# Kernel optimization log

Hardware: AMD Instinct MI355X
Metric: run time of the kernel (lower is better)

The kernel has to match this reference:

```python
import jax, jax.numpy as jnp
import numpy as np

N_NODES = 100000


def gcn_layer(x, W, b, src, dst, norm, n):
    # x: [N, Fin] -> linear transform then normalized scatter-add aggregation
    h = x @ W                                   # [N, Fout]
    msgs = h[src] * norm[:, None]               # [E+N, Fout] edge messages
    out = jax.ops.segment_sum(msgs, dst, num_segments=n)
    return out + b


def _build_graph(edge_index, n):
    # add self loops (PyG GCNConv default)
    loops = jnp.arange(n, dtype=edge_index.dtype)
    src = jnp.concatenate([edge_index[0], loops])
    dst = jnp.concatenate([edge_index[1], loops])
    deg = jax.ops.segment_sum(jnp.ones_like(dst, dtype=jnp.float32), dst, num_segments=n)
    dis = jnp.where(deg > 0, jax.lax.rsqrt(deg), 0.0)  # deg^{-1/2}
    norm = dis[src] * dis[dst]                  # symmetric normalization per edge
    return src, dst, norm


def setup_inputs() -> dict:
    key = jax.random.key(0)
    ks = jax.random.split(key, 8)
    x = jax.random.normal(ks[0], (N_NODES, 3), dtype=jnp.float32)
    edge_index = jax.random.randint(ks[1], (2, 6400000), 0, N_NODES, dtype=jnp.int32)
    def glorot(k, fin, fout):
        s = jnp.sqrt(6.0 / (fin + fout))
        return jax.random.uniform(k, (fin, fout), jnp.float32, -s, s)
    return {
        "x": x,
        "edge_index": edge_index,
        "W1": glorot(ks[2], 3, 32), "b1": jnp.zeros((32,), jnp.float32),
        "W2": glorot(ks[3], 32, 32), "b2": jnp.zeros((32,), jnp.float32),
        "W3": glorot(ks[4], 32, 1), "b3": jnp.zeros((1,), jnp.float32),
    }


def reference(x, edge_index, W1, b1, W2, b2, W3, b3):
    n = x.shape[0]
    src, dst, norm = _build_graph(edge_index, n)
    h = jax.nn.relu(gcn_layer(x, W1, b1, src, dst, norm, n))
    h = jax.nn.relu(gcn_layer(h, W2, b2, src, dst, norm, n))
    return gcn_layer(h, W3, b3, src, dst, norm, n)
```

## Files before the change

### kernel.cpp

```cpp
#include <hip/hip_runtime.h>
#include <hip/hip_fp16.h>


#define BLK 256
#define SB 1280
#define CHUNK 5000
#define BKT 128
#define NBKT 782
#define MAXNB 1024
#define BUFSZ 15360

__global__ void k_hist(const int* __restrict__ dst, int* __restrict__ hist, int E) {
    __shared__ int lh[NBKT];
    for (int b = threadIdx.x; b < NBKT; b += blockDim.x) lh[b] = 0;
    __syncthreads();
    int beg = blockIdx.x * CHUNK;
    int end = min(E, beg + CHUNK);
    int nq = (end - beg) >> 2;
    const int4* d4 = (const int4*)(dst + beg);
    for (int i = threadIdx.x; i < nq; i += blockDim.x) {
        int4 d = d4[i];
        atomicAdd(&lh[d.x >> 7], 1);
        atomicAdd(&lh[d.y >> 7], 1);
        atomicAdd(&lh[d.z >> 7], 1);
        atomicAdd(&lh[d.w >> 7], 1);
    }
    for (int e = beg + (nq << 2) + threadIdx.x; e < end; e += blockDim.x)
        atomicAdd(&lh[dst[e] >> 7], 1);
    __syncthreads();
    for (int b = threadIdx.x; b < NBKT; b += blockDim.x)
        hist[(size_t)blockIdx.x * NBKT + b] = lh[b];
}

__global__ void k_scanA(int* __restrict__ hist, int* __restrict__ btot, int NB) {
    int b = blockIdx.x, t = threadIdx.x;
    int base = t * 5;
    int v0 = hist[(size_t)(base + 0) * NB + b];
    int v1 = hist[(size_t)(base + 1) * NB + b];
    int v2 = hist[(size_t)(base + 2) * NB + b];
    int v3 = hist[(size_t)(base + 3) * NB + b];
    int v4 = hist[(size_t)(base + 4) * NB + b];
    int s = v0 + v1 + v2 + v3 + v4;
    int lane = t & 63, w = t >> 6;
    int x = s;
#pragma unroll
    for (int off = 1; off < 64; off <<= 1) {
        int u = __shfl_up(x, off, 64);
        if (lane >= off) x += u;
    }
    __shared__ int wsum[4];
    if (lane == 63) wsum[w] = x;
    __syncthreads();
    int woff = 0;
    for (int k = 0; k < 4; k++) woff += (k < w) ? wsum[k] : 0;
    int run = woff + x - s;
    hist[(size_t)(base + 0) * NB + b] = run;  run += v0;
    hist[(size_t)(base + 1) * NB + b] = run;  run += v1;
    hist[(size_t)(base + 2) * NB + b] = run;  run += v2;
    hist[(size_t)(base + 3) * NB + b] = run;  run += v3;
    hist[(size_t)(base + 4) * NB + b] = run;  run += v4;
    if (t == 255) btot[b] = run;
}

__global__ void k_scanB(const int* __restrict__ btot, int* __restrict__ bbase,
                        int NB, int E) {
    __shared__ int sh[MAXNB];
    int t = threadIdx.x;
    int v = (t < NB) ? btot[t] : 0;
    sh[t] = v;
    __syncthreads();
    for (int off = 1; off < MAXNB; off <<= 1) {
        int u = (t >= off) ? sh[t - off] : 0;
        __syncthreads();
        sh[t] += u;
        __syncthreads();
    }
    if (t < NB) bbase[t] = sh[t] - v;
    if (t == 0) bbase[NB] = E;
}

__global__ void k_bsort(const int* __restrict__ src, const int* __restrict__ dst,
                        const int* __restrict__ hist, const int* __restrict__ bbase,
                        unsigned int* __restrict__ packed, int E) {
    __shared__ unsigned int bufB[CHUNK];
    __shared__ unsigned short binarr2[CHUNK];
    __shared__ int cnt[NBKT];
    __shared__ int off[NBKT];
    __shared__ int cur[NBKT];
    __shared__ int gbase[NBKT];
    __shared__ int wsum[4];
    int t = threadIdx.x;
    int beg = blockIdx.x * CHUNK;
    int end = min(E, beg + CHUNK);
    int len = end - beg;
    for (int b = t; b < NBKT; b += blockDim.x) {
        cnt[b] = 0;
        gbase[b] = bbase[b] + hist[(size_t)blockIdx.x * NBKT + b];
    }
    __syncthreads();
    {
        int nq = len >> 2;
        const int4* d4 = (const int4*)(dst + beg);
        for (int i = t; i < nq; i += blockDim.x) {
            int4 d = d4[i];
            atomicAdd(&cnt[d.x >> 7], 1);
            atomicAdd(&cnt[d.y >> 7], 1);
            atomicAdd(&cnt[d.z >> 7], 1);
            atomicAdd(&cnt[d.w >> 7], 1);
        }
        for (int i = (nq << 2) + t; i < len; i += blockDim.x)
            atomicAdd(&cnt[dst[beg + i] >> 7], 1);
    }
    __syncthreads();
    {
        int base = t * 4;
        int v0 = (base + 0 < NBKT) ? cnt[base + 0] : 0;
        int v1 = (base + 1 < NBKT) ? cnt[base + 1] : 0;
        int v2 = (base + 2 < NBKT) ? cnt[base + 2] : 0;
        int v3 = (base + 3 < NBKT) ? cnt[base + 3] : 0;
        int s = v0 + v1 + v2 + v3;
        int lane = t & 63, w = t >> 6;
        int x = s;
#pragma unroll
        for (int o = 1; o < 64; o <<= 1) {
            int u = __shfl_up(x, o, 64);
            if (lane >= o) x += u;
        }
        if (lane == 63) wsum[w] = x;
        __syncthreads();
        int woff = 0;
        for (int k = 0; k < 4; k++) woff += (k < w) ? wsum[k] : 0;
        int run = woff + x - s;
        if (base + 0 < NBKT) { off[base + 0] = run; cur[base + 0] = run; } run += v0;
        if (base + 1 < NBKT) { off[base + 1] = run; cur[base + 1] = run; } run += v1;
        if (base + 2 < NBKT) { off[base + 2] = run; cur[base + 2] = run; } run += v2;
        if (base + 3 < NBKT) { off[base + 3] = run; cur[base + 3] = run; } run += v3;
    }
    __syncthreads();
    for (int i = t; i < len; i += blockDim.x) {
        int d = dst[beg + i];
        int s = src[beg + i];
        int b = d >> 7;
        int pos = atomicAdd(&cur[b], 1);
        bufB[pos] = (unsigned)s | ((unsigned)(d & 127) << 17);
        binarr2[pos] = (unsigned short)b;
    }
    __syncthreads();
    for (int i = t; i < len; i += blockDim.x) {
        int b = binarr2[i];
        packed[gbase[b] + i - off[b]] = bufB[i];
    }
}

__global__ void k_sort(unsigned int* __restrict__ packed, const int* __restrict__ bbase,
                       const float* __restrict__ x, float* __restrict__ dis,
                       float4* __restrict__ y4, int* __restrict__ rowptr, int N, int E) {
    __shared__ unsigned int buf[BUFSZ];
    __shared__ int cnt[BKT];
    __shared__ int sc[BKT];
    __shared__ int cur[BKT];
    int b = blockIdx.x, t = threadIdx.x;
    int beg = bbase[b], end = bbase[b + 1];
    int len = end - beg;
    for (int i = t; i < len; i += blockDim.x) buf[i] = packed[beg + i];
    if (t < BKT) cnt[t] = 0;
    __syncthreads();
    for (int i = t; i < len; i += blockDim.x)
        atomicAdd(&cnt[buf[i] >> 17], 1);
    __syncthreads();
    int v = 0;
    if (t < BKT) { v = cnt[t]; sc[t] = v; }
    __syncthreads();
    for (int off = 1; off < BKT; off <<= 1) {
        int u = 0;
        if (t < BKT && t >= off) u = sc[t - off];
        __syncthreads();
        if (t < BKT) sc[t] += u;
        __syncthreads();
    }
    if (t < BKT) {
        int excl = sc[t] - v;
        cur[t] = excl;
        int gi = b * BKT + t;
        if (gi < N) {
            rowptr[gi] = beg + excl;
            float di = rsqrtf((float)v + 1.0f);
            dis[gi] = di;
            float4 y;
            y.x = di * x[3 * gi + 0];
            y.y = di * x[3 * gi + 1];
            y.z = di * x[3 * gi + 2];
            y.w = 0.0f;
            y4[gi] = y;
        }
    }
    __syncthreads();
    for (int i = t; i < len; i += blockDim.x) {
        unsigned vv = buf[i];
        int pos = atomicAdd(&cur[vv >> 17], 1);
        packed[beg + pos] = vv & 0x1FFFF;
    }
    if (b == 0 && t == 0) rowptr[N] = E;
}

__global__ void k_l1(const unsigned int* __restrict__ csr, const int* __restrict__ rowptr,
                     const float4* __restrict__ y4, const float* __restrict__ dis,
                     const float* __restrict__ W1, const float* __restrict__ b1,
                     __half* __restrict__ g, int N) {
    int t = blockIdx.x * blockDim.x + threadIdx.x;
    int i = t >> 5, j = t & 31;
    if (i >= N) return;
    int beg = rowptr[i], end = rowptr[i + 1];
    float ax = 0.f, ay = 0.f, az = 0.f;
    for (int e = beg + j; e < end; e += 32) {
        float4 yv = y4[csr[e]];
        ax += yv.x; ay += yv.y; az += yv.z;
    }
#pragma unroll
    for (int m = 16; m >= 1; m >>= 1) {
        ax += __shfl_xor(ax, m, 32);
        ay += __shfl_xor(ay, m, 32);
        az += __shfl_xor(az, m, 32);
    }
    float di = dis[i];
    float4 ys = y4[i];
    float a0 = di * (ax + ys.x);
    float a1 = di * (ay + ys.y);
    float a2 = di * (az + ys.z);
    float h = b1[j] + a0 * W1[j] + a1 * W1[32 + j] + a2 * W1[64 + j];
    g[(size_t)i * 32 + j] = __float2half(di * fmaxf(h, 0.f));
}

__global__ void k_l2(const unsigned int* __restrict__ csr, const int* __restrict__ rowptr,
                     const __half2* __restrict__ g2, const float* __restrict__ dis,
                     const float* __restrict__ W2, const float* __restrict__ b2,
                     const float* __restrict__ W3, float* __restrict__ q, int N) {
    int t = blockIdx.x * blockDim.x + threadIdx.x;
    int i = t >> 4, j = t & 15;
    if (i >= N) return;
    int beg = rowptr[i], end = rowptr[i + 1];
    float ax0 = 0.f, ay0 = 0.f, ax1 = 0.f, ay1 = 0.f;
    float ax2 = 0.f, ay2 = 0.f, ax3 = 0.f, ay3 = 0.f;
    float ax4 = 0.f, ay4 = 0.f, ax5 = 0.f, ay5 = 0.f;
    float ax6 = 0.f, ay6 = 0.f, ax7 = 0.f, ay7 = 0.f;
    for (int k0 = beg; k0 < end; k0 += 16) {
        int e = k0 + j;
        int myedge = (e < end) ? (int)csr[e] : 0;
        int cnt = min(16, end - k0);
        int t2 = 0;
        for (; t2 + 8 <= cnt; t2 += 8) {
            int s0 = __shfl(myedge, t2 + 0, 16);
            int s1 = __shfl(myedge, t2 + 1, 16);
            int s2 = __shfl(myedge, t2 + 2, 16);
            int s3 = __shfl(myedge, t2 + 3, 16);
            int s4 = __shfl(myedge, t2 + 4, 16);
            int s5 = __shfl(myedge, t2 + 5, 16);
            int s6 = __shfl(myedge, t2 + 6, 16);
            int s7 = __shfl(myedge, t2 + 7, 16);
            float2 f0 = __half22float2(g2[(size_t)s0 * 16 + j]);
            float2 f1 = __half22float2(g2[(size_t)s1 * 16 + j]);
            float2 f2 = __half22float2(g2[(size_t)s2 * 16 + j]);
            float2 f3 = __half22float2(g2[(size_t)s3 * 16 + j]);
            float2 f4 = __half22float2(g2[(size_t)s4 * 16 + j]);
            float2 f5 = __half22float2(g2[(size_t)s5 * 16 + j]);
            float2 f6 = __half22float2(g2[(size_t)s6 * 16 + j]);
            float2 f7 = __half22float2(g2[(size_t)s7 * 16 + j]);
            ax0 += f0.x; ay0 += f0.y;
            ax1 += f1.x; ay1 += f1.y;
            ax2 += f2.x; ay2 += f2.y;
            ax3 += f3.x; ay3 += f3.y;
            ax4 += f4.x; ay4 += f4.y;
            ax5 += f5.x; ay5 += f5.y;
            ax6 += f6.x; ay6 += f6.y;
            ax7 += f7.x; ay7 += f7.y;
        }
        for (; t2 < cnt; t2++) {
            int s = __shfl(myedge, t2, 16);
            float2 f = __half22float2(g2[(size_t)s * 16 + j]);
            ax0 += f.x; ay0 += f.y;
        }
    }
    float accx = ((ax0 + ax1) + (ax2 + ax3)) + ((ax4 + ax5) + (ax6 + ax7));
    float accy = ((ay0 + ay1) + (ay2 + ay3)) + ((ay4 + ay5) + (ay6 + ay7));
    float di = dis[i];
    float2 selfv = __half22float2(g2[(size_t)i * 16 + j]);
    float aX = di * (accx + selfv.x);
    float aY = di * (accy + selfv.y);
    const float2* W2v = (const float2*)W2;
    float ox = b2[2 * j], oy = b2[2 * j + 1];
#pragma unroll
    for (int kk = 0; kk < 16; kk++) {
        float avx = __shfl(aX, kk, 16);
        float avy = __shfl(aY, kk, 16);
        float2 w0 = W2v[(2 * kk) * 16 + j];
        float2 w1 = W2v[(2 * kk + 1) * 16 + j];
        ox += avx * w0.x + avy * w1.x;
        oy += avx * w0.y + avy * w1.y;
    }
    float h2x = fmaxf(ox, 0.f), h2y = fmaxf(oy, 0.f);
    float c = h2x * W3[2 * j] + h2y * W3[2 * j + 1];
#pragma unroll
    for (int m = 8; m >= 1; m >>= 1)
        c += __shfl_xor(c, m, 16);
    if (j == 0) q[i] = di * c;
}

__global__ void k_l3(const unsigned int* __restrict__ csr, const int* __restrict__ rowptr,
                     const float* __restrict__ q, const float* __restrict__ dis,
                     const float* __restrict__ b3, float* __restrict__ out, int N) {
    int t = blockIdx.x * blockDim.x + threadIdx.x;
    int i = t >> 5, j = t & 31;
    if (i >= N) return;
    int beg = rowptr[i], end = rowptr[i + 1];
    float acc = 0.f;
    for (int e = beg + j; e < end; e += 32)
        acc += q[csr[e]];
#pragma unroll
    for (int m = 16; m >= 1; m >>= 1)
        acc += __shfl_xor(acc, m, 32);
    if (j == 0) out[i] = dis[i] * (acc + q[i]) + b3[0];
}

extern "C" void kernel_launch(void* const* d_in, const int* in_sizes, int n_in,
                              void* d_out, int out_size, void* d_ws, size_t ws_size,
                              hipStream_t stream) {
    const float* x  = (const float*)d_in[0];
    const int*   ei = (const int*)d_in[1];
    const float* W1 = (const float*)d_in[2];
    const float* b1 = (const float*)d_in[3];
    const float* W2 = (const float*)d_in[4];
    const float* b2 = (const float*)d_in[5];
    const float* W3 = (const float*)d_in[6];
    const float* b3 = (const float*)d_in[7];
    float* out = (float*)d_out;

    int N = in_sizes[0] / 3;
    int E = in_sizes[1] / 2;
    const int* src = ei;
    const int* dst = ei + E;

    char* w = (char*)d_ws;
    int*   hist   = (int*)w;       w += (size_t)SB * NBKT * 4;
    int*   btot   = (int*)w;       w += (size_t)MAXNB * 4;
    int*   bbase  = (int*)w;       w += (size_t)(MAXNB + 1) * 4;
    int*   rowptr = (int*)w;       w += (size_t)(N + 1) * 4;
    float* dis    = (float*)w;     w += (size_t)N * 4;
    float* y4     = (float*)w;     w += (size_t)N * 16;
    __half* g     = (__half*)w;    w += (size_t)N * 32 * 2;
    float* q      = (float*)w;     w += (size_t)N * 4;
    unsigned int* packed = (unsigned int*)w;  w += (size_t)E * 4;

    k_hist <<<SB, BLK, 0, stream>>>(dst, hist, E);
    k_scanA<<<NBKT, BLK, 0, stream>>>(hist, btot, NBKT);
    k_scanB<<<1, MAXNB, 0, stream>>>(btot, bbase, NBKT, E);
    k_bsort<<<SB, BLK, 0, stream>>>(src, dst, hist, bbase, packed, E);
    k_sort <<<NBKT, BLK, 0, stream>>>(packed, bbase, x, dis, (float4*)y4, rowptr, N, E);

    long long tn32 = (long long)N * 32;
    unsigned gn32 = (unsigned)((tn32 + BLK - 1) / BLK);
    long long tn16 = (long long)N * 16;
    unsigned gn16 = (unsigned)((tn16 + BLK - 1) / BLK);
    k_l1<<<gn32, BLK, 0, stream>>>(packed, rowptr, (const float4*)y4, dis, W1, b1, g, N);
    k_l2<<<gn16, BLK, 0, stream>>>(packed, rowptr, (const __half2*)g, dis, W2, b2, W3, q, N);
    k_l3<<<gn32, BLK, 0, stream>>>(packed, rowptr, q, dis, b3, out, N);
}
```

Measured before the change: 375.1 us.

## Split layer-2 aggregation into two feature-half passes for cache-resident gathers

Layer-1 output is written as two separate 16-feature half tables, and the layer-2 aggregation runs twice, once per half, with 8 lanes per node. Each gather table is half the size (about 3.2MB instead of 6.4MB), so random gathers are more likely to hit in L2. A separate kernel then applies W2, ReLU and W3 to the combined partial sums. In exchange, the CSR index array is read twice, and extra float partial buffers are written and read back. Nontemporal loads and stores are also used for the CSR stream and the partials.

```diff
diff --git a/kernel.cpp b/kernel.cpp
--- a/kernel.cpp
+++ b/kernel.cpp
@@ -206,7 +206,7 @@
 __global__ void k_l1(const unsigned int* __restrict__ csr, const int* __restrict__ rowptr,
                      const float4* __restrict__ y4, const float* __restrict__ dis,
                      const float* __restrict__ W1, const float* __restrict__ b1,
-                     __half* __restrict__ g, int N) {
+                     __half* __restrict__ gA, __half* __restrict__ gB, int N) {
     int t = blockIdx.x * blockDim.x + threadIdx.x;
     int i = t >> 5, j = t & 31;
     if (i >= N) return;
@@ -228,43 +228,43 @@
     float a1 = di * (ay + ys.y);
     float a2 = di * (az + ys.z);
     float h = b1[j] + a0 * W1[j] + a1 * W1[32 + j] + a2 * W1[64 + j];
-    g[(size_t)i * 32 + j] = __float2half(di * fmaxf(h, 0.f));
-}
-
-__global__ void k_l2(const unsigned int* __restrict__ csr, const int* __restrict__ rowptr,
-                     const __half2* __restrict__ g2, const float* __restrict__ dis,
-                     const float* __restrict__ W2, const float* __restrict__ b2,
-                     const float* __restrict__ W3, float* __restrict__ q, int N) {
+    __half hv = __float2half(di * fmaxf(h, 0.f));
+    if (j < 16) gA[(size_t)i * 16 + j] = hv;
+    else        gB[(size_t)i * 16 + (j - 16)] = hv;
+}
+
+__global__ void k_l2a(const unsigned int* __restrict__ csr, const int* __restrict__ rowptr,
+                      const __half2* __restrict__ gh, const float* __restrict__ dis,
+                      float* __restrict__ part, int N) {
     int t = blockIdx.x * blockDim.x + threadIdx.x;
-    int i = t >> 4, j = t & 15;
+    int i = t >> 3, j = t & 7;
     if (i >= N) return;
     int beg = rowptr[i], end = rowptr[i + 1];
     float ax0 = 0.f, ay0 = 0.f, ax1 = 0.f, ay1 = 0.f;
     float ax2 = 0.f, ay2 = 0.f, ax3 = 0.f, ay3 = 0.f;
     float ax4 = 0.f, ay4 = 0.f, ax5 = 0.f, ay5 = 0.f;
     float ax6 = 0.f, ay6 = 0.f, ax7 = 0.f, ay7 = 0.f;
-    for (int k0 = beg; k0 < end; k0 += 16) {
+    for (int k0 = beg; k0 < end; k0 += 8) {
         int e = k0 + j;
-        int myedge = (e < end) ? (int)csr[e] : 0;
-        int cnt = min(16, end - k0);
-        int t2 = 0;
-        for (; t2 + 8 <= cnt; t2 += 8) {
-            int s0 = __shfl(myedge, t2 + 0, 16);
-            int s1 = __shfl(myedge, t2 + 1, 16);
-            int s2 = __shfl(myedge, t2 + 2, 16);
-            int s3 = __shfl(myedge, t2 + 3, 16);
-            int s4 = __shfl(myedge, t2 + 4, 16);
-            int s5 = __shfl(myedge, t2 + 5, 16);
-            int s6 = __shfl(myedge, t2 + 6, 16);
-            int s7 = __shfl(myedge, t2 + 7, 16);
-            float2 f0 = __half22float2(g2[(size_t)s0 * 16 + j]);
-            float2 f1 = __half22float2(g2[(size_t)s1 * 16 + j]);
-            float2 f2 = __half22float2(g2[(size_t)s2 * 16 + j]);
-            float2 f3 = __half22float2(g2[(size_t)s3 * 16 + j]);
-            float2 f4 = __half22float2(g2[(size_t)s4 * 16 + j]);
-            float2 f5 = __half22float2(g2[(size_t)s5 * 16 + j]);
-            float2 f6 = __half22float2(g2[(size_t)s6 * 16 + j]);
-            float2 f7 = __half22float2(g2[(size_t)s7 * 16 + j]);
+        int myedge = (e < end) ? (int)__builtin_nontemporal_load(&csr[e]) : 0;
+        int cnt = min(8, end - k0);
+        if (cnt == 8) {
+            int s0 = __shfl(myedge, 0, 8);
+            int s1 = __shfl(myedge, 1, 8);
+            int s2 = __shfl(myedge, 2, 8);
+            int s3 = __shfl(myedge, 3, 8);
+            int s4 = __shfl(myedge, 4, 8);
+            int s5 = __shfl(myedge, 5, 8);
+            int s6 = __shfl(myedge, 6, 8);
+            int s7 = __shfl(myedge, 7, 8);
+            float2 f0 = __half22float2(gh[(size_t)s0 * 8 + j]);
+            float2 f1 = __half22float2(gh[(size_t)s1 * 8 + j]);
+            float2 f2 = __half22float2(gh[(size_t)s2 * 8 + j]);
+            float2 f3 = __half22float2(gh[(size_t)s3 * 8 + j]);
+            float2 f4 = __half22float2(gh[(size_t)s4 * 8 + j]);
+            float2 f5 = __half22float2(gh[(size_t)s5 * 8 + j]);
+            float2 f6 = __half22float2(gh[(size_t)s6 * 8 + j]);
+            float2 f7 = __half22float2(gh[(size_t)s7 * 8 + j]);
             ax0 += f0.x; ay0 += f0.y;
             ax1 += f1.x; ay1 += f1.y;
             ax2 += f2.x; ay2 += f2.y;
@@ -273,19 +273,33 @@
             ax5 += f5.x; ay5 += f5.y;
             ax6 += f6.x; ay6 += f6.y;
             ax7 += f7.x; ay7 += f7.y;
-        }
-        for (; t2 < cnt; t2++) {
-            int s = __shfl(myedge, t2, 16);
-            float2 f = __half22float2(g2[(size_t)s * 16 + j]);
-            ax0 += f.x; ay0 += f.y;
+        } else {
+            for (int t2 = 0; t2 < cnt; t2++) {
+                int s = __shfl(myedge, t2, 8);
+                float2 f = __half22float2(gh[(size_t)s * 8 + j]);
+                ax0 += f.x; ay0 += f.y;
+            }
         }
     }
     float accx = ((ax0 + ax1) + (ax2 + ax3)) + ((ax4 + ax5) + (ax6 + ax7));
     float accy = ((ay0 + ay1) + (ay2 + ay3)) + ((ay4 + ay5) + (ay6 + ay7));
     float di = dis[i];
-    float2 selfv = __half22float2(g2[(size_t)i * 16 + j]);
-    float aX = di * (accx + selfv.x);
-    float aY = di * (accy + selfv.y);
+    float2 selfv = __half22float2(gh[(size_t)i * 8 + j]);
+    size_t o = ((size_t)i * 8 + j) * 2;
+    __builtin_nontemporal_store(di * (accx + selfv.x), &part[o]);
+    __builtin_nontemporal_store(di * (accy + selfv.y), &part[o + 1]);
+}
+
+__global__ void k_l2b(const float2* __restrict__ partA, const float2* __restrict__ partB,
+                      const float* __restrict__ dis,
+                      const float* __restrict__ W2, const float* __restrict__ b2,
+                      const float* __restrict__ W3, float* __restrict__ q, int N) {
+    int t = blockIdx.x * blockDim.x + threadIdx.x;
+    int i = t >> 4, j = t & 15;
+    if (i >= N) return;
+    const float2* part = (j < 8) ? partA : partB;
+    float2 a = part[(size_t)i * 8 + (j & 7)];
+    float aX = a.x, aY = a.y;
     const float2* W2v = (const float2*)W2;
     float ox = b2[2 * j], oy = b2[2 * j + 1];
 #pragma unroll
@@ -302,7 +316,7 @@
 #pragma unroll
     for (int m = 8; m >= 1; m >>= 1)
         c += __shfl_xor(c, m, 16);
-    if (j == 0) q[i] = di * c;
+    if (j == 0) q[i] = dis[i] * c;
 }
 
 __global__ void k_l3(const unsigned int* __restrict__ csr, const int* __restrict__ rowptr,
@@ -346,7 +360,10 @@
     int*   rowptr = (int*)w;       w += (size_t)(N + 1) * 4;
     float* dis    = (float*)w;     w += (size_t)N * 4;
     float* y4     = (float*)w;     w += (size_t)N * 16;
-    __half* g     = (__half*)w;    w += (size_t)N * 32 * 2;
+    __half* gA    = (__half*)w;    w += (size_t)N * 16 * 2;
+    __half* gB    = (__half*)w;    w += (size_t)N * 16 * 2;
+    float* partA  = (float*)w;     w += (size_t)N * 16 * 4;
+    float* partB  = (float*)w;     w += (size_t)N * 16 * 4;
     float* q      = (float*)w;     w += (size_t)N * 4;
     unsigned int* packed = (unsigned int*)w;  w += (size_t)E * 4;
 
@@ -360,7 +377,12 @@
     unsigned gn32 = (unsigned)((tn32 + BLK - 1) / BLK);
     long long tn16 = (long long)N * 16;
     unsigned gn16 = (unsigned)((tn16 + BLK - 1) / BLK);
-    k_l1<<<gn32, BLK, 0, stream>>>(packed, rowptr, (const float4*)y4, dis, W1, b1, g, N);
-    k_l2<<<gn16, BLK, 0, stream>>>(packed, rowptr, (const __half2*)g, dis, W2, b2, W3, q, N);
-    k_l3<<<gn32, BLK, 0, stream>>>(packed, rowptr, q, dis, b3, out, N);
-}
+    long long tn8 = (long long)N * 8;
+    unsigned gn8 = (unsigned)((tn8 + BLK - 1) / BLK);
+
+    k_l1 <<<gn32, BLK, 0, stream>>>(packed, rowptr, (const float4*)y4, dis, W1, b1, gA, gB, N);
+    k_l2a<<<gn8,  BLK, 0, stream>>>(packed, rowptr, (const __half2*)gA, dis, partA, N);
+    k_l2a<<<gn8,  BLK, 0, stream>>>(packed, rowptr, (const __half2*)gB, dis, partB, N);
+    k_l2b<<<gn16, BLK, 0, stream>>>((const float2*)partA, (const float2*)partB, dis, W2, b2, W3, q, N);
+    k_l3 <<<gn32, BLK, 0, stream>>>(packed, rowptr, q, dis, b3, out, N);
+}
```

Result: slower. 463.0 us (+23.4%).
